# Kernel tuning notes

Measured on AMD Instinct MI355X. Metric: run time of the kernel, lower is better.

Reference implementation:

```python
import jax, jax.numpy as jnp
import numpy as np

EPS = 1e-5

def setup_inputs() -> dict:
    key = jax.random.key(0)
    ks = jax.random.split(key, 10)
    B, C, H, W = 32, 512, 64, 64
    Cr = C // 16
    s = lambda n: 1.0 / np.sqrt(n)
    return {
        "x": jax.random.normal(ks[0], (B, C, H, W), jnp.float32),
        "w_mask": jax.random.normal(ks[1], (C,), jnp.float32) * s(C),   # conv_mask weight [1,C,1,1] -> [C]
        "b_mask": jax.random.normal(ks[2], (), jnp.float32) * 0.01,
        "w1": jax.random.normal(ks[3], (Cr, C), jnp.float32) * s(C),    # 1x1 conv C->Cr
        "b1": jax.random.normal(ks[4], (Cr,), jnp.float32) * 0.01,
        "ln_g": jnp.ones((Cr,), jnp.float32),
        "ln_b": jnp.zeros((Cr,), jnp.float32),
        "w2": jax.random.normal(ks[5], (C, Cr), jnp.float32) * s(Cr),   # 1x1 conv Cr->C
        "b2": jax.random.normal(ks[6], (C,), jnp.float32) * 0.01,
    }

def reference(x, w_mask, b_mask, w1, b1, ln_g, ln_b, w2, b2):
    B, C, H, W = x.shape
    xf = x.reshape(B, C, H * W)                                    # [B,C,HW]
    # spatial attention pooling (1x1 conv -> softmax over HW -> weighted sum)
    logits = jnp.einsum('bchw,c->bhw', x, w_mask).reshape(B, H * W) + b_mask
    attn = jax.nn.softmax(logits, axis=-1)                         # [B,HW]
    context = jnp.einsum('bcs,bs->bc', xf, attn)                   # [B,C]
    # bottleneck MLP gate: conv1 -> LayerNorm over Cr -> ReLU -> conv2 -> sigmoid
    t = context @ w1.T + b1                                        # [B,Cr]
    mu = jnp.mean(t, axis=-1, keepdims=True)
    var = jnp.mean(jnp.square(t - mu), axis=-1, keepdims=True)
    t = (t - mu) * jax.lax.rsqrt(var + EPS) * ln_g + ln_b
    t = jax.nn.relu(t)
    gate = jax.nn.sigmoid(t @ w2.T + b2)[:, :, None, None]         # [B,C,1,1]
    # instance norm (no affine, biased var over HW)
    m = jnp.mean(xf, axis=-1, keepdims=True)
    v = jnp.mean(jnp.square(xf - m), axis=-1, keepdims=True)
    xn = ((xf - m) * jax.lax.rsqrt(v + EPS)).reshape(B, C, H, W)
    return x * gate + (1.0 - gate) * xn
```

## Files before the change

kernel.cpp:

```cpp
#include <hip/hip_runtime.h>
#include <math.h>

#define B_   32
#define C_   512
#define CR_  32
#define HW_  4096
#define NCH  16
#define CPB  (C_/NCH)
#define EPSV 1e-5f

typedef float v4f __attribute__((ext_vector_type(4)));

__device__ inline ushort bf16_rne(float f) {
    const unsigned u = __float_as_uint(f);
    return (ushort)((u + 0x7fffu + ((u >> 16) & 1u)) >> 16);
}
__device__ inline float bf16_up(ushort h) {
    return __uint_as_float(((unsigned)h) << 16);
}

__global__ __launch_bounds__(256) void k1_logits_echo(
    const float* __restrict__ x, const float* __restrict__ w_mask,
    float* __restrict__ partial, ushort* __restrict__ xh)
{
    const int b = blockIdx.y, ch = blockIdx.x, t = threadIdx.x;
    const int s0 = blockIdx.z * 512;
    const int c0 = ch * CPB;
    v4f a0 = {0,0,0,0}, a1 = {0,0,0,0};
#pragma unroll 4
    for (int cc = 0; cc < CPB; ++cc) {
        const int c = c0 + cc;
        const float w = w_mask[c];
        const v4f* px = reinterpret_cast<const v4f*>(x + (size_t)(b * C_ + c) * HW_) + s0;
        const v4f v0 = __builtin_nontemporal_load(px + t);
        const v4f v1 = __builtin_nontemporal_load(px + t + 256);
        a0 += w * v0;
        a1 += w * v1;
        ushort4* ph = reinterpret_cast<ushort4*>(xh + (size_t)(b * C_ + c) * HW_) + s0;
        ushort4 h0, h1;
        h0.x = bf16_rne(v0.x); h0.y = bf16_rne(v0.y); h0.z = bf16_rne(v0.z); h0.w = bf16_rne(v0.w);
        h1.x = bf16_rne(v1.x); h1.y = bf16_rne(v1.y); h1.z = bf16_rne(v1.z); h1.w = bf16_rne(v1.w);
        ph[t      ] = h0;
        ph[t + 256] = h1;
    }
    v4f* pp = reinterpret_cast<v4f*>(partial + (size_t)(b * NCH + ch) * HW_) + s0;
    pp[t      ] = a0;
    pp[t + 256] = a1;
}

__global__ __launch_bounds__(256) void k2_softmax(
    const float* __restrict__ partial, float* __restrict__ attn)
{
    __shared__ float l4[4];
    __shared__ float sM, sZ;
    const int b = blockIdx.x, t = threadIdx.x;
    const int lane = t & 63, wid = t >> 6;
    float4 v[4];
#pragma unroll
    for (int k = 0; k < 4; ++k) {
        float4 s = {0,0,0,0};
        const int i = t + 256 * k;
#pragma unroll
        for (int ch = 0; ch < NCH; ++ch) {
            const float4 p = reinterpret_cast<const float4*>(partial + (size_t)(b * NCH + ch) * HW_)[i];
            s.x += p.x; s.y += p.y; s.z += p.z; s.w += p.w;
        }
        v[k] = s;
    }
    float mx = -3.0e38f;
#pragma unroll
    for (int k = 0; k < 4; ++k)
        mx = fmaxf(mx, fmaxf(fmaxf(v[k].x, v[k].y), fmaxf(v[k].z, v[k].w)));
#pragma unroll
    for (int o = 32; o > 0; o >>= 1) mx = fmaxf(mx, __shfl_down(mx, o));
    if (lane == 0) l4[wid] = mx;
    __syncthreads();
    if (t == 0) sM = fmaxf(fmaxf(l4[0], l4[1]), fmaxf(l4[2], l4[3]));
    __syncthreads();
    const float M = sM;
    float e[16];
    float sum = 0.f;
#pragma unroll
    for (int k = 0; k < 4; ++k) {
        e[k*4+0] = expf(v[k].x - M);
        e[k*4+1] = expf(v[k].y - M);
        e[k*4+2] = expf(v[k].z - M);
        e[k*4+3] = expf(v[k].w - M);
        sum += e[k*4+0] + e[k*4+1] + e[k*4+2] + e[k*4+3];
    }
#pragma unroll
    for (int o = 32; o > 0; o >>= 1) sum += __shfl_down(sum, o);
    __syncthreads();
    if (lane == 0) l4[wid] = sum;
    __syncthreads();
    if (t == 0) sZ = l4[0] + l4[1] + l4[2] + l4[3];
    __syncthreads();
    const float rz = 1.f / sZ;
    float4* pa = reinterpret_cast<float4*>(attn + (size_t)b * HW_);
#pragma unroll
    for (int k = 0; k < 4; ++k)
        pa[t + 256 * k] = make_float4(e[k*4+0]*rz, e[k*4+1]*rz, e[k*4+2]*rz, e[k*4+3]*rz);
}

__global__ __launch_bounds__(256) void k3_context_stats(
    const ushort* __restrict__ xh, const float* __restrict__ attn,
    float* __restrict__ ctx, float* __restrict__ sums, float* __restrict__ sqs)
{
    __shared__ float ld[12];
    const int b = blockIdx.y, c = blockIdx.x, t = threadIdx.x;
    const int lane = t & 63, wid = t >> 6;
    const ushort4* ph = reinterpret_cast<const ushort4*>(xh + (size_t)(b * C_ + c) * HW_);
    const float4* pa = reinterpret_cast<const float4*>(attn + (size_t)b * HW_);
    float dot = 0.f, sm = 0.f, sq = 0.f;
#pragma unroll
    for (int k = 0; k < 4; ++k) {
        const ushort4 h = ph[t + 256 * k];
        const float4 av = pa[t + 256 * k];
        const float x0 = bf16_up(h.x), x1 = bf16_up(h.y), x2 = bf16_up(h.z), x3 = bf16_up(h.w);
        dot += x0*av.x + x1*av.y + x2*av.z + x3*av.w;
        sm  += x0 + x1 + x2 + x3;
        sq  += x0*x0 + x1*x1 + x2*x2 + x3*x3;
    }
#pragma unroll
    for (int o = 32; o > 0; o >>= 1) {
        dot += __shfl_down(dot, o);
        sm  += __shfl_down(sm, o);
        sq  += __shfl_down(sq, o);
    }
    if (lane == 0) { ld[wid] = dot; ld[4 + wid] = sm; ld[8 + wid] = sq; }
    __syncthreads();
    if (t == 0) {
        ctx [b * C_ + c] = ld[0] + ld[1] + ld[2]  + ld[3];
        sums[b * C_ + c] = ld[4] + ld[5] + ld[6]  + ld[7];
        sqs [b * C_ + c] = ld[8] + ld[9] + ld[10] + ld[11];
    }
}

__global__ __launch_bounds__(256) void k4_mlp(
    const float* __restrict__ ctx, const float* __restrict__ w1, const float* __restrict__ b1,
    const float* __restrict__ ln_g, const float* __restrict__ ln_b,
    const float* __restrict__ w2, const float* __restrict__ b2,
    const float* __restrict__ sums, const float* __restrict__ sqs,
    float* __restrict__ Ab, float* __restrict__ Db)
{
    __shared__ float cs[C_];
    __shared__ float tl[CR_];
    const int b = blockIdx.x, t = threadIdx.x;
    cs[t]       = ctx[b * C_ + t];
    cs[t + 256] = ctx[b * C_ + t + 256];
    __syncthreads();

    const int row = t >> 3, sub = t & 7;
    float p = 0.f;
#pragma unroll 8
    for (int k = 0; k < 64; ++k) {
        const int c = sub + (k << 3);
        p += cs[c] * w1[row * C_ + c];
    }
    p += __shfl_down(p, 4, 8);
    p += __shfl_down(p, 2, 8);
    p += __shfl_down(p, 1, 8);
    if (sub == 0) tl[row] = p + b1[row];
    __syncthreads();

    float tn = 0.f;
    if (t < CR_) {
        float mu = 0.f;
#pragma unroll
        for (int i = 0; i < CR_; ++i) mu += tl[i];
        mu *= (1.f / CR_);
        float var = 0.f;
#pragma unroll
        for (int i = 0; i < CR_; ++i) { const float d = tl[i] - mu; var += d * d; }
        var *= (1.f / CR_);
        tn = (tl[t] - mu) * rsqrtf(var + EPSV) * ln_g[t] + ln_b[t];
        tn = fmaxf(tn, 0.f);
    }
    __syncthreads();
    if (t < CR_) tl[t] = tn;
    __syncthreads();

#pragma unroll
    for (int r = 0; r < 2; ++r) {
        const int c = t + r * 256;
        float g = b2[c];
#pragma unroll
        for (int i = 0; i < CR_; ++i) g += tl[i] * w2[c * CR_ + i];
        g = 1.f / (1.f + expf(-g));
        const float m  = sums[b * C_ + c] * (1.f / HW_);
        const float v  = sqs [b * C_ + c] * (1.f / HW_) - m * m;
        const float rn = rsqrtf(v + EPSV);
        Ab[b * C_ + c] = g + (1.f - g) * rn;
        Db[b * C_ + c] = -(1.f - g) * rn * m;
    }
}

__global__ __launch_bounds__(256) void k5_apply(
    const ushort* __restrict__ xh, const float* __restrict__ Ab, const float* __restrict__ Db,
    float* __restrict__ out)
{
    const int b = blockIdx.y, c = blockIdx.x, t = threadIdx.x;
    const size_t base = (size_t)(b * C_ + c) * HW_;
    const float a = Ab[b * C_ + c], d = Db[b * C_ + c];
    const ushort4* ph = reinterpret_cast<const ushort4*>(xh + base);
    v4f*           po = reinterpret_cast<v4f*>(out + base);
#pragma unroll
    for (int k = 0; k < 4; ++k) {
        const ushort4 h = ph[t + 256 * k];
        v4f r;
        r.x = fmaf(a, bf16_up(h.x), d); r.y = fmaf(a, bf16_up(h.y), d);
        r.z = fmaf(a, bf16_up(h.z), d); r.w = fmaf(a, bf16_up(h.w), d);
        __builtin_nontemporal_store(r, po + t + 256 * k);
    }
}

extern "C" void kernel_launch(void* const* d_in, const int* in_sizes, int n_in,
                              void* d_out, int out_size, void* d_ws, size_t ws_size,
                              hipStream_t stream)
{
    const float* x      = (const float*)d_in[0];
    const float* w_mask = (const float*)d_in[1];
    const float* w1     = (const float*)d_in[3];
    const float* b1     = (const float*)d_in[4];
    const float* ln_g   = (const float*)d_in[5];
    const float* ln_b   = (const float*)d_in[6];
    const float* w2     = (const float*)d_in[7];
    const float* b2     = (const float*)d_in[8];
    float* out = (float*)d_out;

    float* ws      = (float*)d_ws;
    float* partial = ws;
    float* attn    = partial + (size_t)B_ * NCH * HW_;
    float* ctx     = attn   + B_ * HW_;
    float* sums    = ctx    + B_ * C_;
    float* sqs     = sums   + B_ * C_;
    float* Ab      = sqs    + B_ * C_;
    float* Db      = Ab     + B_ * C_;
    ushort* xh     = (ushort*)(Db + B_ * C_);

    k1_logits_echo<<<dim3(NCH, B_, 2), 256, 0, stream>>>(x, w_mask, partial, xh);
    k2_softmax<<<B_, 256, 0, stream>>>(partial, attn);
    k3_context_stats<<<dim3(C_, B_), 256, 0, stream>>>(xh, attn, ctx, sums, sqs);
    k4_mlp<<<B_, 256, 0, stream>>>(ctx, w1, b1, ln_g, ln_b, w2, b2, sums, sqs, Ab, Db);
    k5_apply<<<dim3(C_, B_), 256, 0, stream>>>(xh, Ab, Db, out);
}
```

Before: 170.3 us.

## Fuse softmax and MLP into producer kernels via last-block atomic counters

Folds the softmax into the logits/bf16-echo kernel and the bottleneck MLP into the context/stats kernel. Each uses a per-batch atomic counter so the last finishing block does the batch-wide reduction. This removes two separate low-occupancy launches and their inter-kernel gaps. In exchange it adds agent-scope atomic stores and loads, a memset for the counters, and a serialized tail done by one block per batch. K5 also switches to nontemporal loads of the bf16 copy.

```diff
diff --git a/kernel.cpp b/kernel.cpp
--- a/kernel.cpp
+++ b/kernel.cpp
@@ -9,23 +9,41 @@
 #define CPB  (C_/NCH)
 #define EPSV 1e-5f
 
-typedef float v4f __attribute__((ext_vector_type(4)));
+typedef float          v4f __attribute__((ext_vector_type(4)));
+typedef unsigned short v4h __attribute__((ext_vector_type(4)));
 
 __device__ inline ushort bf16_rne(float f) {
     const unsigned u = __float_as_uint(f);
     return (ushort)((u + 0x7fffu + ((u >> 16) & 1u)) >> 16);
 }
-__device__ inline float bf16_up(ushort h) {
-    return __uint_as_float(((unsigned)h) << 16);
-}
-
-__global__ __launch_bounds__(256) void k1_logits_echo(
+__device__ inline float bf16_up(ushort h) { return __uint_as_float(((unsigned)h) << 16); }
+
+__device__ inline void st_u64_agent(unsigned long long* p, unsigned long long v) {
+    __hip_atomic_store(p, v, __ATOMIC_RELAXED, __HIP_MEMORY_SCOPE_AGENT);
+}
+__device__ inline unsigned long long ld_u64_agent(const unsigned long long* p) {
+    return __hip_atomic_load(p, __ATOMIC_RELAXED, __HIP_MEMORY_SCOPE_AGENT);
+}
+__device__ inline void st_f32_agent(float* p, float v) {
+    __hip_atomic_store(p, v, __ATOMIC_RELAXED, __HIP_MEMORY_SCOPE_AGENT);
+}
+__device__ inline float ld_f32_agent(const float* p) {
+    return __hip_atomic_load(p, __ATOMIC_RELAXED, __HIP_MEMORY_SCOPE_AGENT);
+}
+
+__global__ __launch_bounds__(256) void K1_logits_echo_softmax(
     const float* __restrict__ x, const float* __restrict__ w_mask,
-    float* __restrict__ partial, ushort* __restrict__ xh)
-{
+    float* __restrict__ partial, ushort* __restrict__ xh,
+    float* __restrict__ attn, int* __restrict__ cnt)
+{
+    __shared__ float l4[4];
+    __shared__ float sMZ;
+    __shared__ int   isLastS;
     const int b = blockIdx.y, ch = blockIdx.x, t = threadIdx.x;
     const int s0 = blockIdx.z * 512;
     const int c0 = ch * CPB;
+    const int lane = t & 63, wid = t >> 6;
+
     v4f a0 = {0,0,0,0}, a1 = {0,0,0,0};
 #pragma unroll 4
     for (int cc = 0; cc < CPB; ++cc) {
@@ -36,85 +54,94 @@
         const v4f v1 = __builtin_nontemporal_load(px + t + 256);
         a0 += w * v0;
         a1 += w * v1;
-        ushort4* ph = reinterpret_cast<ushort4*>(xh + (size_t)(b * C_ + c) * HW_) + s0;
-        ushort4 h0, h1;
+        v4h h0, h1;
         h0.x = bf16_rne(v0.x); h0.y = bf16_rne(v0.y); h0.z = bf16_rne(v0.z); h0.w = bf16_rne(v0.w);
         h1.x = bf16_rne(v1.x); h1.y = bf16_rne(v1.y); h1.z = bf16_rne(v1.z); h1.w = bf16_rne(v1.w);
+        v4h* ph = reinterpret_cast<v4h*>(xh + (size_t)(b * C_ + c) * HW_) + s0;
         ph[t      ] = h0;
         ph[t + 256] = h1;
     }
-    v4f* pp = reinterpret_cast<v4f*>(partial + (size_t)(b * NCH + ch) * HW_) + s0;
-    pp[t      ] = a0;
-    pp[t + 256] = a1;
-}
-
-__global__ __launch_bounds__(256) void k2_softmax(
-    const float* __restrict__ partial, float* __restrict__ attn)
-{
-    __shared__ float l4[4];
-    __shared__ float sM, sZ;
-    const int b = blockIdx.x, t = threadIdx.x;
-    const int lane = t & 63, wid = t >> 6;
-    float4 v[4];
-#pragma unroll
-    for (int k = 0; k < 4; ++k) {
-        float4 s = {0,0,0,0};
+
+    unsigned long long* pp =
+        reinterpret_cast<unsigned long long*>(partial + (size_t)(b * NCH + ch) * HW_) + 2 * s0;
+    union { v4f f; unsigned long long u[2]; } q0, q1;
+    q0.f = a0; q1.f = a1;
+    st_u64_agent(pp + 2*t,           q0.u[0]);
+    st_u64_agent(pp + 2*t + 1,       q0.u[1]);
+    st_u64_agent(pp + 2*(t+256),     q1.u[0]);
+    st_u64_agent(pp + 2*(t+256) + 1, q1.u[1]);
+
+    __syncthreads();
+    if (t == 0) {
+        const int old = __hip_atomic_fetch_add(&cnt[b], 1,
+                            __ATOMIC_ACQ_REL, __HIP_MEMORY_SCOPE_AGENT);
+        isLastS = (old == 2 * NCH - 1);
+    }
+    __syncthreads();
+    if (!isLastS) return;
+
+    float va[16];
+    const unsigned long long* pb =
+        reinterpret_cast<const unsigned long long*>(partial + (size_t)b * NCH * HW_);
+#pragma unroll
+    for (int k = 0; k < 8; ++k) {
         const int i = t + 256 * k;
-#pragma unroll
-        for (int ch = 0; ch < NCH; ++ch) {
-            const float4 p = reinterpret_cast<const float4*>(partial + (size_t)(b * NCH + ch) * HW_)[i];
-            s.x += p.x; s.y += p.y; s.z += p.z; s.w += p.w;
+        float sa = 0.f, sb = 0.f;
+#pragma unroll
+        for (int c2 = 0; c2 < NCH; ++c2) {
+            union { unsigned long long u; float f[2]; } w2;
+            w2.u = ld_u64_agent(pb + (size_t)c2 * (HW_ / 2) + i);
+            sa += w2.f[0]; sb += w2.f[1];
         }
-        v[k] = s;
+        va[2*k] = sa; va[2*k+1] = sb;
     }
     float mx = -3.0e38f;
 #pragma unroll
-    for (int k = 0; k < 4; ++k)
-        mx = fmaxf(mx, fmaxf(fmaxf(v[k].x, v[k].y), fmaxf(v[k].z, v[k].w)));
+    for (int j = 0; j < 16; ++j) mx = fmaxf(mx, va[j]);
 #pragma unroll
     for (int o = 32; o > 0; o >>= 1) mx = fmaxf(mx, __shfl_down(mx, o));
     if (lane == 0) l4[wid] = mx;
     __syncthreads();
-    if (t == 0) sM = fmaxf(fmaxf(l4[0], l4[1]), fmaxf(l4[2], l4[3]));
-    __syncthreads();
-    const float M = sM;
-    float e[16];
+    if (t == 0) sMZ = fmaxf(fmaxf(l4[0], l4[1]), fmaxf(l4[2], l4[3]));
+    __syncthreads();
+    const float M = sMZ;
     float sum = 0.f;
 #pragma unroll
-    for (int k = 0; k < 4; ++k) {
-        e[k*4+0] = expf(v[k].x - M);
-        e[k*4+1] = expf(v[k].y - M);
-        e[k*4+2] = expf(v[k].z - M);
-        e[k*4+3] = expf(v[k].w - M);
-        sum += e[k*4+0] + e[k*4+1] + e[k*4+2] + e[k*4+3];
-    }
+    for (int j = 0; j < 16; ++j) { va[j] = expf(va[j] - M); sum += va[j]; }
 #pragma unroll
     for (int o = 32; o > 0; o >>= 1) sum += __shfl_down(sum, o);
     __syncthreads();
     if (lane == 0) l4[wid] = sum;
     __syncthreads();
-    if (t == 0) sZ = l4[0] + l4[1] + l4[2] + l4[3];
-    __syncthreads();
-    const float rz = 1.f / sZ;
-    float4* pa = reinterpret_cast<float4*>(attn + (size_t)b * HW_);
-#pragma unroll
-    for (int k = 0; k < 4; ++k)
-        pa[t + 256 * k] = make_float4(e[k*4+0]*rz, e[k*4+1]*rz, e[k*4+2]*rz, e[k*4+3]*rz);
-}
-
-__global__ __launch_bounds__(256) void k3_context_stats(
+    if (t == 0) sMZ = l4[0] + l4[1] + l4[2] + l4[3];
+    __syncthreads();
+    const float rz = 1.f / sMZ;
+    float2* pa = reinterpret_cast<float2*>(attn + (size_t)b * HW_);
+#pragma unroll
+    for (int k = 0; k < 8; ++k)
+        pa[t + 256 * k] = make_float2(va[2*k] * rz, va[2*k+1] * rz);
+}
+
+__global__ __launch_bounds__(256) void K3_ctx_stats_mlp(
     const ushort* __restrict__ xh, const float* __restrict__ attn,
-    float* __restrict__ ctx, float* __restrict__ sums, float* __restrict__ sqs)
+    const float* __restrict__ w1, const float* __restrict__ b1,
+    const float* __restrict__ ln_g, const float* __restrict__ ln_b,
+    const float* __restrict__ w2, const float* __restrict__ b2,
+    float* __restrict__ ctx, float* __restrict__ sums, float* __restrict__ sqs,
+    float* __restrict__ Ab, float* __restrict__ Db, int* __restrict__ cnt)
 {
     __shared__ float ld[12];
+    __shared__ int   isLastS;
+    __shared__ float cs[C_];
+    __shared__ float tl[CR_];
     const int b = blockIdx.y, c = blockIdx.x, t = threadIdx.x;
     const int lane = t & 63, wid = t >> 6;
-    const ushort4* ph = reinterpret_cast<const ushort4*>(xh + (size_t)(b * C_ + c) * HW_);
+    const v4h* ph = reinterpret_cast<const v4h*>(xh + (size_t)(b * C_ + c) * HW_);
     const float4* pa = reinterpret_cast<const float4*>(attn + (size_t)b * HW_);
     float dot = 0.f, sm = 0.f, sq = 0.f;
 #pragma unroll
     for (int k = 0; k < 4; ++k) {
-        const ushort4 h = ph[t + 256 * k];
+        const v4h h = ph[t + 256 * k];
         const float4 av = pa[t + 256 * k];
         const float x0 = bf16_up(h.x), x1 = bf16_up(h.y), x2 = bf16_up(h.z), x3 = bf16_up(h.w);
         dot += x0*av.x + x1*av.y + x2*av.z + x3*av.w;
@@ -130,32 +157,27 @@
     if (lane == 0) { ld[wid] = dot; ld[4 + wid] = sm; ld[8 + wid] = sq; }
     __syncthreads();
     if (t == 0) {
-        ctx [b * C_ + c] = ld[0] + ld[1] + ld[2]  + ld[3];
-        sums[b * C_ + c] = ld[4] + ld[5] + ld[6]  + ld[7];
-        sqs [b * C_ + c] = ld[8] + ld[9] + ld[10] + ld[11];
-    }
-}
-
-__global__ __launch_bounds__(256) void k4_mlp(
-    const float* __restrict__ ctx, const float* __restrict__ w1, const float* __restrict__ b1,
-    const float* __restrict__ ln_g, const float* __restrict__ ln_b,
-    const float* __restrict__ w2, const float* __restrict__ b2,
-    const float* __restrict__ sums, const float* __restrict__ sqs,
-    float* __restrict__ Ab, float* __restrict__ Db)
-{
-    __shared__ float cs[C_];
-    __shared__ float tl[CR_];
-    const int b = blockIdx.x, t = threadIdx.x;
-    cs[t]       = ctx[b * C_ + t];
-    cs[t + 256] = ctx[b * C_ + t + 256];
+        const int idx = b * C_ + c;
+        st_f32_agent(&ctx [idx], ld[0] + ld[1] + ld[2]  + ld[3]);
+        st_f32_agent(&sums[idx], ld[4] + ld[5] + ld[6]  + ld[7]);
+        st_f32_agent(&sqs [idx], ld[8] + ld[9] + ld[10] + ld[11]);
+        const int old = __hip_atomic_fetch_add(&cnt[b], 1,
+                            __ATOMIC_ACQ_REL, __HIP_MEMORY_SCOPE_AGENT);
+        isLastS = (old == C_ - 1);
+    }
+    __syncthreads();
+    if (!isLastS) return;
+
+    cs[t]       = ld_f32_agent(&ctx[b * C_ + t]);
+    cs[t + 256] = ld_f32_agent(&ctx[b * C_ + t + 256]);
     __syncthreads();
 
     const int row = t >> 3, sub = t & 7;
     float p = 0.f;
-#pragma unroll 8
+#pragma unroll 4
     for (int k = 0; k < 64; ++k) {
-        const int c = sub + (k << 3);
-        p += cs[c] * w1[row * C_ + c];
+        const int cc = sub + (k << 3);
+        p += cs[cc] * w1[row * C_ + cc];
     }
     p += __shfl_down(p, 4, 8);
     p += __shfl_down(p, 2, 8);
@@ -182,31 +204,33 @@
 
 #pragma unroll
     for (int r = 0; r < 2; ++r) {
-        const int c = t + r * 256;
-        float g = b2[c];
-#pragma unroll
-        for (int i = 0; i < CR_; ++i) g += tl[i] * w2[c * CR_ + i];
+        const int cc = t + r * 256;
+        float g = b2[cc];
+#pragma unroll 8
+        for (int i = 0; i < CR_; ++i) g += tl[i] * w2[cc * CR_ + i];
         g = 1.f / (1.f + expf(-g));
-        const float m  = sums[b * C_ + c] * (1.f / HW_);
-        const float v  = sqs [b * C_ + c] * (1.f / HW_) - m * m;
+        const float s1 = ld_f32_agent(&sums[b * C_ + cc]);
+        const float s2 = ld_f32_agent(&sqs [b * C_ + cc]);
+        const float m  = s1 * (1.f / HW_);
+        const float v  = s2 * (1.f / HW_) - m * m;
         const float rn = rsqrtf(v + EPSV);
-        Ab[b * C_ + c] = g + (1.f - g) * rn;
-        Db[b * C_ + c] = -(1.f - g) * rn * m;
-    }
-}
-
-__global__ __launch_bounds__(256) void k5_apply(
+        Ab[b * C_ + cc] = g + (1.f - g) * rn;
+        Db[b * C_ + cc] = -(1.f - g) * rn * m;
+    }
+}
+
+__global__ __launch_bounds__(256) void K5_apply(
     const ushort* __restrict__ xh, const float* __restrict__ Ab, const float* __restrict__ Db,
     float* __restrict__ out)
 {
     const int b = blockIdx.y, c = blockIdx.x, t = threadIdx.x;
     const size_t base = (size_t)(b * C_ + c) * HW_;
     const float a = Ab[b * C_ + c], d = Db[b * C_ + c];
-    const ushort4* ph = reinterpret_cast<const ushort4*>(xh + base);
-    v4f*           po = reinterpret_cast<v4f*>(out + base);
+    const v4h* ph = reinterpret_cast<const v4h*>(xh + base);
+    v4f*       po = reinterpret_cast<v4f*>(out + base);
 #pragma unroll
     for (int k = 0; k < 4; ++k) {
-        const ushort4 h = ph[t + 256 * k];
+        const v4h h = __builtin_nontemporal_load(ph + t + 256 * k);
         v4f r;
         r.x = fmaf(a, bf16_up(h.x), d); r.y = fmaf(a, bf16_up(h.y), d);
         r.z = fmaf(a, bf16_up(h.z), d); r.w = fmaf(a, bf16_up(h.w), d);
@@ -237,10 +261,12 @@
     float* Ab      = sqs    + B_ * C_;
     float* Db      = Ab     + B_ * C_;
     ushort* xh     = (ushort*)(Db + B_ * C_);
-
-    k1_logits_echo<<<dim3(NCH, B_, 2), 256, 0, stream>>>(x, w_mask, partial, xh);
-    k2_softmax<<<B_, 256, 0, stream>>>(partial, attn);
-    k3_context_stats<<<dim3(C_, B_), 256, 0, stream>>>(xh, attn, ctx, sums, sqs);
-    k4_mlp<<<B_, 256, 0, stream>>>(ctx, w1, b1, ln_g, ln_b, w2, b2, sums, sqs, Ab, Db);
-    k5_apply<<<dim3(C_, B_), 256, 0, stream>>>(xh, Ab, Db, out);
-}
+    int*   syncbuf = (int*)(xh + (size_t)B_ * C_ * HW_);
+
+    hipMemsetAsync(syncbuf, 0, 2 * B_ * sizeof(int), stream);
+    K1_logits_echo_softmax<<<dim3(NCH, B_, 2), 256, 0, stream>>>(
+        x, w_mask, partial, xh, attn, syncbuf);
+    K3_ctx_stats_mlp<<<dim3(C_, B_), 256, 0, stream>>>(
+        xh, attn, w1, b1, ln_g, ln_b, w2, b2, ctx, sums, sqs, Ab, Db, syncbuf + B_);
+    K5_apply<<<dim3(C_, B_), 256, 0, stream>>>(xh, Ab, Db, out);
+}
```

Result: slower. 626.5 us (+267.8%).
